# Kernel tuning notes

Measured on AMD Instinct MI355X. Metric: run time of the kernel, lower is better.

Reference implementation:

```python
import jax, jax.numpy as jnp
import numpy as np

B, T, N, D, C = 32, 256, 256, 1024, 80
SIM_THRESH = 0.7
MAX_AGE = 10
W_SIM, W_IOU = 0.7, 0.3


def setup_inputs() -> dict:
    key = jax.random.key(0)
    ks = jax.random.split(key, 8)
    track_memory = jax.random.normal(ks[0], (B, T, D), jnp.float32)
    track_boxes = jax.random.uniform(ks[1], (B, T, 4), jnp.float32, 0.05, 0.95)
    track_active = jax.random.bernoulli(ks[2], 0.9, (B, T))
    track_age = jax.random.randint(ks[3], (B, T), 0, 5, jnp.int32)
    track_hits = jax.random.randint(ks[4], (B, T), 1, 10, jnp.int32)
    det_boxes = jax.random.uniform(ks[5], (B, N, 4), jnp.float32, 0.05, 0.95)
    # correlate detections with tracks so cosine similarity exceeds the
    # matching threshold for many pairs and the greedy loop does real work
    det_memory = track_memory + 0.3 * jax.random.normal(ks[6], (B, N, D), jnp.float32)
    class_logits = jax.random.normal(ks[7], (B, N, C), jnp.float32)
    return {
        'track_memory': track_memory, 'track_boxes': track_boxes,
        'track_active': track_active, 'track_age': track_age,
        'track_hits': track_hits, 'det_boxes': det_boxes,
        'det_memory': det_memory, 'class_logits': class_logits,
    }


def _normalize(x):
    # matches F.normalize(dim=-1): x / max(||x||, eps)
    n = jnp.linalg.norm(x, axis=-1, keepdims=True)
    return x / jnp.maximum(n, 1e-12)


def _iou_matrix(tb, db):
    # tb [T,4], db [N,4], boxes in (cx, cy, w, h) format -> IoU [T,N]
    t_x1, t_y1 = tb[:, 0] - tb[:, 2] / 2, tb[:, 1] - tb[:, 3] / 2
    t_x2, t_y2 = tb[:, 0] + tb[:, 2] / 2, tb[:, 1] + tb[:, 3] / 2
    d_x1, d_y1 = db[:, 0] - db[:, 2] / 2, db[:, 1] - db[:, 3] / 2
    d_x2, d_y2 = db[:, 0] + db[:, 2] / 2, db[:, 1] + db[:, 3] / 2
    iw = jnp.clip(jnp.minimum(t_x2[:, None], d_x2[None, :]) - jnp.maximum(t_x1[:, None], d_x1[None, :]), 0.0)
    ih = jnp.clip(jnp.minimum(t_y2[:, None], d_y2[None, :]) - jnp.maximum(t_y1[:, None], d_y1[None, :]), 0.0)
    inter = iw * ih
    union = (tb[:, 2] * tb[:, 3])[:, None] + (db[:, 2] * db[:, 3])[None, :] - inter
    return inter / (union + 1e-6)


def _greedy_match(Cmat):
    # sequential greedy argmax matching, as in the torch while-loop.
    # returns match_det [T]: detection index matched to each track, -1 if none.
    Tn, Nn = Cmat.shape

    def step(carry, _):
        Cm, match_det = carry
        flat = Cm.reshape(-1)
        idx = jnp.argmax(flat)
        val = flat[idx]
        ok = val >= SIM_THRESH
        t = idx // Nn
        d = idx % Nn
        match_det = jnp.where(ok, match_det.at[t].set(d.astype(jnp.int32)), match_det)
        Cm = jnp.where(ok, Cm.at[t, :].set(-1.0).at[:, d].set(-1.0), Cm)
        return (Cm, match_det), None

    init = (Cmat, jnp.full((Tn,), -1, jnp.int32))
    (_, match_det), _ = jax.lax.scan(step, init, None, length=min(Tn, Nn))
    return match_det


def reference(track_memory, track_boxes, track_active, track_age, track_hits,
              det_boxes, det_memory, class_logits):
    # detection scores (computed in torch update(); not used downstream)
    scores = jnp.max(jax.nn.softmax(class_logits, axis=-1), axis=-1)  # [B,N]

    def per_batch(tm, tb, ta, age, hits, db, dm):
        sim = _normalize(tm) @ _normalize(dm).T            # [T,N] cosine sim
        iou = _iou_matrix(tb, db)                          # [T,N]
        Cmat = W_SIM * sim + W_IOU * iou
        Cmat = jnp.where(ta[:, None], Cmat, -1.0)          # inactive rows -> -1
        match_det = _greedy_match(Cmat)                    # [T]
        matched = match_det >= 0
        d = jnp.clip(match_det, 0)
        new_mem = jnp.where(matched[:, None], dm[d], tm)
        new_box = jnp.where(matched[:, None], db[d], tb)
        new_hits = jnp.where(matched, hits + 1, hits)
        unmatched_active = ta & ~matched
        new_age = jnp.where(matched, 0, jnp.where(unmatched_active, age + 1, age))
        new_active = jnp.where(matched, True,
                               jnp.where(unmatched_active, new_age <= MAX_AGE, ta))
        return new_mem, new_box, new_active, new_age, new_hits, match_det

    new_mem, new_box, new_active, new_age, new_hits, match_det = jax.vmap(per_batch)(
        track_memory, track_boxes, track_active, track_age, track_hits,
        det_boxes, det_memory)
    return new_mem, new_box, new_active, new_age, new_hits, match_det, scores
```

## Files before the change

### kernel.cpp

```cpp
#include <hip/hip_runtime.h>
#include <math.h>

static constexpr int PB = 32, PT = 256, PN = 256, PD = 1024, PC = 80;
static constexpr int BCAP = 96;
static constexpr int CAP  = 256;
static constexpr int NT   = 16;

static constexpr size_t O_MEM   = 0;
static constexpr size_t O_BOX   = O_MEM   + (size_t)PB*PT*PD;
static constexpr size_t O_ACT   = O_BOX   + (size_t)PB*PT*4;
static constexpr size_t O_AGE   = O_ACT   + (size_t)PB*PT;
static constexpr size_t O_HITS  = O_AGE   + (size_t)PB*PT;
static constexpr size_t O_MATCH = O_HITS  + (size_t)PB*PT;
static constexpr size_t O_SCORE = O_MATCH + (size_t)PB*PT;

typedef __attribute__((ext_vector_type(8))) short short8;
typedef __attribute__((ext_vector_type(4))) float f32x4;

__device__ __forceinline__ unsigned ordbits(float f) {
    unsigned b = __float_as_uint(f);
    return (b & 0x80000000u) ? ~b : (b | 0x80000000u);
}
__device__ __forceinline__ unsigned short f2bf(float f) {
    unsigned u = __float_as_uint(f);
    unsigned r = u + 0x7fffu + ((u >> 16) & 1u);
    return (unsigned short)(r >> 16);
}

__device__ __forceinline__ float box_cost(float sim, float4 bt, float4 bd) {
    float tX1 = bt.x - bt.z*0.5f, tX2 = bt.x + bt.z*0.5f;
    float tY1 = bt.y - bt.w*0.5f, tY2 = bt.y + bt.w*0.5f;
    float dX1 = bd.x - bd.z*0.5f, dX2 = bd.x + bd.z*0.5f;
    float dY1 = bd.y - bd.w*0.5f, dY2 = bd.y + bd.w*0.5f;
    float iw = fmaxf(fminf(tX2, dX2) - fmaxf(tX1, dX1), 0.f);
    float ih = fmaxf(fminf(tY2, dY2) - fmaxf(tY1, dY1), 0.f);
    float inter = iw * ih;
    float iou = inter / (bt.z*bt.w + bd.z*bd.w - inter + 1e-6f);
    return 0.7f * sim + 0.3f * iou;
}

__global__ __launch_bounds__(256) void k_prep(
        const float* __restrict__ tm, const float* __restrict__ dm,
        const float* __restrict__ lg,
        short* __restrict__ abf, short* __restrict__ bbf,
        float* __restrict__ asums, float* __restrict__ bsums,
        float* __restrict__ ddots, float* __restrict__ out) {
    const int bx = blockIdx.x;
    const int tid = threadIdx.x;
    const int w = tid >> 6, lane = tid & 63;
    if (bx < PB * PT / 4) {
        const size_t row = (size_t)bx * 4 + w;
        const float4* ap = (const float4*)(tm + row * PD);
        const float4* dp = (const float4*)(dm + row * PD);
        float4 a[4], d[4];
#pragma unroll
        for (int q = 0; q < 4; ++q) { a[q] = ap[lane + 64 * q]; d[q] = dp[lane + 64 * q]; }
        float as = 0.f, bs = 0.f, dd = 0.f;
        uint2 pa[4], pd2[4];
#pragma unroll
        for (int q = 0; q < 4; ++q) {
            as += a[q].x*a[q].x + a[q].y*a[q].y + a[q].z*a[q].z + a[q].w*a[q].w;
            bs += d[q].x*d[q].x + d[q].y*d[q].y + d[q].z*d[q].z + d[q].w*d[q].w;
            dd += a[q].x*d[q].x + a[q].y*d[q].y + a[q].z*d[q].z + a[q].w*d[q].w;
            pa[q].x  = f2bf(a[q].x) | ((unsigned)f2bf(a[q].y) << 16);
            pa[q].y  = f2bf(a[q].z) | ((unsigned)f2bf(a[q].w) << 16);
            pd2[q].x = f2bf(d[q].x) | ((unsigned)f2bf(d[q].y) << 16);
            pd2[q].y = f2bf(d[q].z) | ((unsigned)f2bf(d[q].w) << 16);
        }
        uint2* ao = (uint2*)(abf + row * PD);
        uint2* bo = (uint2*)(bbf + row * PD);
#pragma unroll
        for (int q = 0; q < 4; ++q) { ao[lane + 64 * q] = pa[q]; bo[lane + 64 * q] = pd2[q]; }
#pragma unroll
        for (int o = 1; o < 64; o <<= 1) {
            as += __shfl_xor(as, o);
            bs += __shfl_xor(bs, o);
            dd += __shfl_xor(dd, o);
        }
        if (lane == 0) {
            asums[row] = as;
            bsums[row] = bs;
            ddots[row] = dd;
        }
    } else {
        int rowi = (bx - PB * PT / 4) * 4 + w;
        const float* p = lg + (size_t)rowi * PC;
        float x0 = p[lane];
        float x1 = (lane < PC - 64) ? p[64 + lane] : -INFINITY;
        float m = fmaxf(x0, x1);
#pragma unroll
        for (int o = 32; o > 0; o >>= 1) m = fmaxf(m, __shfl_down(m, o));
        m = __shfl(m, 0);
        float s = expf(x0 - m) + ((lane < PC - 64) ? expf(x1 - m) : 0.f);
#pragma unroll
        for (int o = 32; o > 0; o >>= 1) s += __shfl_down(s, o);
        if (lane == 0) out[O_SCORE + rowi] = 1.0f / s;
    }
}

__global__ __launch_bounds__(256) void k_sim(
        const short* __restrict__ abf, const short* __restrict__ bbf,
        const float* __restrict__ tb, const float* __restrict__ db,
        const unsigned* __restrict__ ta,
        const float* __restrict__ asums, const float* __restrict__ bsums,
        unsigned* __restrict__ cntblk, int* __restrict__ cand) {
    const int b = blockIdx.z;
    const int rowbase = blockIdx.y * 64;
    const int colbase = blockIdx.x * 64;
    const int bid = b * NT + blockIdx.y * 4 + blockIdx.x;
    const int tid = threadIdx.x;
    const int w = tid >> 6, lane = tid & 63;
    const int wm = w >> 1, wn = w & 1;
    const int m16 = lane & 15, quad = lane >> 4;

    __shared__ unsigned bcnt;
    __shared__ float ainv[64], binv[64];
    if (tid == 0) bcnt = 0u;
    if (tid < 64)
        ainv[tid] = 1.0f / fmaxf(sqrtf(asums[b * PT + rowbase + tid]), 1e-12f);
    else if (tid < 128)
        binv[tid - 64] = 1.0f / fmaxf(sqrtf(bsums[b * PN + colbase + tid - 64]), 1e-12f);

    const short* Ab = abf + ((size_t)b * PT + rowbase) * PD;
    const short* Bb = bbf + ((size_t)b * PN + colbase) * PD;
    const short8* pA0 = (const short8*)(Ab + (size_t)(wm * 32 +      m16) * PD) + quad;
    const short8* pA1 = (const short8*)(Ab + (size_t)(wm * 32 + 16 + m16) * PD) + quad;
    const short8* pB0 = (const short8*)(Bb + (size_t)(wn * 32 +      m16) * PD) + quad;
    const short8* pB1 = (const short8*)(Bb + (size_t)(wn * 32 + 16 + m16) * PD) + quad;

    f32x4 acc00 = (f32x4)0.f, acc01 = (f32x4)0.f;
    f32x4 acc10 = (f32x4)0.f, acc11 = (f32x4)0.f;
#pragma unroll 8
    for (int kk = 0; kk < PD / 32; ++kk) {
        short8 a0 = pA0[kk * 4];
        short8 a1 = pA1[kk * 4];
        short8 b0 = pB0[kk * 4];
        short8 b1 = pB1[kk * 4];
        acc00 = __builtin_amdgcn_mfma_f32_16x16x32_bf16(a0, b0, acc00, 0, 0, 0);
        acc01 = __builtin_amdgcn_mfma_f32_16x16x32_bf16(a0, b1, acc01, 0, 0, 0);
        acc10 = __builtin_amdgcn_mfma_f32_16x16x32_bf16(a1, b0, acc10, 0, 0, 0);
        acc11 = __builtin_amdgcn_mfma_f32_16x16x32_bf16(a1, b1, acc11, 0, 0, 0);
    }
    f32x4 accm[2][2] = {{acc00, acc01}, {acc10, acc11}};

    __syncthreads();

    float dx1[2], dy1[2], dx2[2], dy2[2], darea[2], dnv[2];
    int ng[2];
#pragma unroll
    for (int nj = 0; nj < 2; ++nj) {
        int cl = wn * 32 + nj * 16 + m16;
        ng[nj] = colbase + cl;
        dnv[nj] = binv[cl];
        float4 bx = *(const float4*)&db[((size_t)b * PN + ng[nj]) * 4];
        dx1[nj] = bx.x - bx.z * 0.5f; dx2[nj] = bx.x + bx.z * 0.5f;
        dy1[nj] = bx.y - bx.w * 0.5f; dy2[nj] = bx.y + bx.w * 0.5f;
        darea[nj] = bx.z * bx.w;
    }

#pragma unroll
    for (int mi = 0; mi < 2; ++mi) {
#pragma unroll
        for (int r = 0; r < 4; ++r) {
            int tl = wm * 32 + mi * 16 + quad * 4 + r;
            int tg = rowbase + tl;
            if (ta[b * PT + tg] == 0u) continue;
            float tnv = ainv[tl];
            float4 bx = *(const float4*)&tb[((size_t)b * PT + tg) * 4];
            float tX1 = bx.x - bx.z * 0.5f, tX2 = bx.x + bx.z * 0.5f;
            float tY1 = bx.y - bx.w * 0.5f, tY2 = bx.y + bx.w * 0.5f;
            float tA = bx.z * bx.w;
#pragma unroll
            for (int nj = 0; nj < 2; ++nj) {
                float sim = accm[mi][nj][r] * tnv * dnv[nj];
                float iw = fmaxf(fminf(tX2, dx2[nj]) - fmaxf(tX1, dx1[nj]), 0.f);
                float ih = fmaxf(fminf(tY2, dy2[nj]) - fmaxf(tY1, dy1[nj]), 0.f);
                float inter = iw * ih;
                float iou = inter / (tA + darea[nj] - inter + 1e-6f);
                float cost = 0.7f * sim + 0.3f * iou;
                if (cost >= 0.695f) {
                    unsigned idx = atomicAdd(&bcnt, 1u);
                    if (idx < BCAP) cand[bid * BCAP + idx] = (tg << 8) | ng[nj];
                }
            }
        }
    }
    __syncthreads();
    if (tid == 0) cntblk[bid] = (bcnt > BCAP) ? BCAP : bcnt;
}

__global__ __launch_bounds__(256) void k_match(
        const float* __restrict__ tm, const float* __restrict__ dm,
        const float* __restrict__ tb, const float* __restrict__ db,
        const float* __restrict__ asums, const float* __restrict__ bsums,
        const float* __restrict__ ddots,
        const unsigned* __restrict__ cntblk, const int* __restrict__ cand,
        int* __restrict__ md) {
    const int b = blockIdx.x;
    const int tid = threadIdx.x;
    const int w = tid >> 6, lane = tid & 63;
    __shared__ int cnts[NT];
    __shared__ unsigned long long sel_key[CAP];
    __shared__ unsigned sel_cnt;
    __shared__ int odd_slot[64];
    __shared__ unsigned odd_cnt;
    __shared__ int rcnt[PT];
    __shared__ int ccnt[PN];
    __shared__ int conflict;

    if (tid == 0) { sel_cnt = 0u; odd_cnt = 0u; conflict = 0; }
    if (tid < NT) {
        int cj = (int)cntblk[b * NT + tid];
        cnts[tid] = (cj > BCAP) ? BCAP : cj;
    }
    rcnt[tid] = 0; ccnt[tid] = 0;
    md[b * PT + tid] = -1;
    __syncthreads();

    for (int u = tid; u < NT * BCAP; u += 256) {
        int j = u / BCAP, i = u - j * BCAP;
        if (i >= cnts[j]) continue;
        int gidx = (b * NT + j) * BCAP + i;
        int pair = cand[gidx];
        int t = pair >> 8, n = pair & 255;
        if (t == n) {
            float na  = asums[b * PT + t];
            float nb  = bsums[b * PN + n];
            float dot = ddots[b * PT + t];
            float sim = dot * (1.0f / fmaxf(sqrtf(na), 1e-12f))
                            * (1.0f / fmaxf(sqrtf(nb), 1e-12f));
            float4 bt = *(const float4*)&tb[((size_t)b * PT + t) * 4];
            float4 bd = *(const float4*)&db[((size_t)b * PN + n) * 4];
            float cost = box_cost(sim, bt, bd);
            if (cost >= 0.7f) {
                unsigned s = atomicAdd(&sel_cnt, 1u);
                if (s < CAP)
                    sel_key[s] = ((unsigned long long)ordbits(cost) << 16)
                               | (unsigned long long)(65535 - pair);
            }
        } else {
            unsigned oi = atomicAdd(&odd_cnt, 1u);
            if (oi < 64) odd_slot[oi] = gidx;
        }
    }
    __syncthreads();

    int nodd = (int)odd_cnt; if (nodd > 64) nodd = 64;
    for (int j = w; j < nodd; j += 4) {
        int pair = cand[odd_slot[j]];
        int t = pair >> 8, n = pair & 255;
        const float4* tr = (const float4*)(tm + ((size_t)b * PT + t) * PD);
        const float4* dr = (const float4*)(dm + ((size_t)b * PN + n) * PD);
        float dot = 0.f;
#pragma unroll
        for (int q = 0; q < 4; ++q) {
            float4 v = tr[lane + 64 * q];
            float4 u = dr[lane + 64 * q];
            dot += v.x*u.x + v.y*u.y + v.z*u.z + v.w*u.w;
        }
#pragma unroll
        for (int o = 1; o < 64; o <<= 1) dot += __shfl_xor(dot, o);
        if (lane == 0) {
            float na = asums[b * PT + t], nb = bsums[b * PN + n];
            float sim = dot * (1.0f / fmaxf(sqrtf(na), 1e-12f))
                            * (1.0f / fmaxf(sqrtf(nb), 1e-12f));
            float4 bt = *(const float4*)&tb[((size_t)b * PT + t) * 4];
            float4 bd = *(const float4*)&db[((size_t)b * PN + n) * 4];
            float cost = box_cost(sim, bt, bd);
            if (cost >= 0.7f) {
                unsigned s = atomicAdd(&sel_cnt, 1u);
                if (s < CAP)
                    sel_key[s] = ((unsigned long long)ordbits(cost) << 16)
                               | (unsigned long long)(65535 - pair);
            }
        }
    }
    __syncthreads();

    const unsigned ns = (sel_cnt > (unsigned)CAP) ? (unsigned)CAP : sel_cnt;
    for (unsigned s = tid; s < ns; s += 256) {
        int flat = 65535 - (int)(sel_key[s] & 0xFFFFull);
        if (atomicAdd(&rcnt[flat >> 8], 1) >= 1) conflict = 1;
        if (atomicAdd(&ccnt[flat & 255], 1) >= 1) conflict = 1;
    }
    __syncthreads();

    if (!conflict) {
        for (unsigned s = tid; s < ns; s += 256) {
            int flat = 65535 - (int)(sel_key[s] & 0xFFFFull);
            md[b * PT + (flat >> 8)] = flat & 255;
        }
        return;
    }

    if (w == 0) {
        unsigned long long k[4];
#pragma unroll
        for (int s = 0; s < 4; ++s) {
            unsigned idx = (unsigned)lane + 64u * s;
            k[s] = (idx < ns) ? sel_key[idx] : 0ull;
        }
        int mdv[4] = {-1, -1, -1, -1};
        for (int it = 0; it < PT; ++it) {
            unsigned long long m = k[0];
            if (k[1] > m) m = k[1];
            if (k[2] > m) m = k[2];
            if (k[3] > m) m = k[3];
#pragma unroll
            for (int o = 1; o < 64; o <<= 1) {
                unsigned long long s = __shfl_xor(m, o);
                if (s > m) m = s;
            }
            if (m == 0ull) break;
            int flat = 65535 - (int)(m & 0xFFFFull);
            int t = flat >> 8, d = flat & 255;
            if ((t & 63) == lane) mdv[t >> 6] = d;
#pragma unroll
            for (int s = 0; s < 4; ++s) {
                if (k[s]) {
                    int f2 = 65535 - (int)(k[s] & 0xFFFFull);
                    if ((f2 >> 8) == t || (f2 & 255) == d) k[s] = 0ull;
                }
            }
        }
#pragma unroll
        for (int s = 0; s < 4; ++s) md[b * PT + s * 64 + lane] = mdv[s];
    }
}

__global__ __launch_bounds__(256) void k_outsc(
        const float* __restrict__ tm, const float* __restrict__ tb,
        const unsigned* __restrict__ ta, const int* __restrict__ age,
        const int* __restrict__ hits, const float* __restrict__ db,
        const float* __restrict__ dm, const int* __restrict__ md,
        float* __restrict__ out) {
    const int w = threadIdx.x >> 6, lane = threadIdx.x & 63;
    int idx = blockIdx.x * 4 + w;
    int b = idx >> 8;
    int m = md[idx];
    bool matched = m >= 0;
    int d = matched ? m : 0;
    const float4* src = (const float4*)(matched ? dm + ((size_t)b * PN + d) * PD
                                                : tm + (size_t)idx * PD);
    float4* dst = (float4*)(out + O_MEM + (size_t)idx * PD);
#pragma unroll
    for (int q = 0; q < 4; ++q) dst[lane + 64 * q] = src[lane + 64 * q];
    if (lane < 4) {
        const float* sb = matched ? db + ((size_t)b * PN + d) * 4
                                  : tb + (size_t)idx * 4;
        out[O_BOX + (size_t)idx * 4 + lane] = sb[lane];
    }
    if (lane == 0) {
        bool tact = ta[idx] != 0u;
        int hh = hits[idx], ag = age[idx];
        int nh = matched ? hh + 1 : hh;
        bool unm = tact && !matched;
        int na = matched ? 0 : (unm ? ag + 1 : ag);
        bool nact = matched ? true : (unm ? (na <= 10) : tact);
        out[O_ACT   + idx] = nact ? 1.0f : 0.0f;
        out[O_AGE   + idx] = (float)na;
        out[O_HITS  + idx] = (float)nh;
        out[O_MATCH + idx] = (float)m;
    }
}

extern "C" void kernel_launch(void* const* d_in, const int* in_sizes, int n_in,
                              void* d_out, int out_size, void* d_ws, size_t ws_size,
                              hipStream_t stream) {
    const float*    tm   = (const float*)d_in[0];
    const float*    tb   = (const float*)d_in[1];
    const unsigned* ta   = (const unsigned*)d_in[2];
    const int*      age  = (const int*)d_in[3];
    const int*      hits = (const int*)d_in[4];
    const float*    db   = (const float*)d_in[5];
    const float*    dm   = (const float*)d_in[6];
    const float*    lg   = (const float*)d_in[7];
    float* out = (float*)d_out;

    char* ws = (char*)d_ws;
    short* abf   = (short*)ws;
    short* bbf   = abf + (size_t)PB * PT * PD;
    float* asums = (float*)(bbf + (size_t)PB * PN * PD);
    float* bsums = asums + PB * PT;
    float* ddots = bsums + PB * PN;
    unsigned* cntblk = (unsigned*)(ddots + PB * PT);
    int* cand = (int*)(cntblk + PB * NT);
    int* md   = cand + PB * NT * BCAP;

    k_prep <<<PB * PT / 4 + PB * PN / 4, 256, 0, stream>>>(
        tm, dm, lg, abf, bbf, asums, bsums, ddots, out);
    k_sim  <<<dim3(4, 4, PB), 256, 0, stream>>>(
        abf, bbf, tb, db, ta, asums, bsums, cntblk, cand);
    k_match<<<dim3(PB), 256, 0, stream>>>(
        tm, dm, tb, db, asums, bsums, ddots, cntblk, cand, md);
    k_outsc<<<PB * PT / 4, 256, 0, stream>>>(
        tm, tb, ta, age, hits, db, dm, md, out);
}
```

Baseline: 169.6 us.

## Store bf16 operands in MFMA fragment order and remap sim blocks per XCD

The prep kernel now writes the bf16 copies of track and detection memory pre-swizzled into 16-row MFMA fragment tiles, so each lane of k_sim reads a contiguous short8 and a wave's loads are fully coalesced instead of strided across rows. Row norms and dot products are reduced across waves through shared memory because each block now handles 16 rows. k_sim uses a 1D grid with batches mapped to XCDs so the tiles of one batch share an L2. This couples the prep and sim kernels to a fixed fragment layout and makes k_prep launch fewer, heavier blocks for that part.

```diff
diff --git a/kernel.cpp b/kernel.cpp
--- a/kernel.cpp
+++ b/kernel.cpp
@@ -17,6 +17,7 @@
 typedef __attribute__((ext_vector_type(8))) short short8;
 typedef __attribute__((ext_vector_type(4))) float f32x4;
 
+
 __device__ __forceinline__ unsigned ordbits(float f) {
     unsigned b = __float_as_uint(f);
     return (b & 0x80000000u) ? ~b : (b | 0x80000000u);
@@ -25,6 +26,14 @@
     unsigned u = __float_as_uint(f);
     unsigned r = u + 0x7fffu + ((u >> 16) & 1u);
     return (unsigned short)(r >> 16);
+}
+__device__ __forceinline__ short8 pack8(float4 lo, float4 hi) {
+    union { unsigned u[4]; short8 s; } r;
+    r.u[0] = f2bf(lo.x) | ((unsigned)f2bf(lo.y) << 16);
+    r.u[1] = f2bf(lo.z) | ((unsigned)f2bf(lo.w) << 16);
+    r.u[2] = f2bf(hi.x) | ((unsigned)f2bf(hi.y) << 16);
+    r.u[3] = f2bf(hi.z) | ((unsigned)f2bf(hi.w) << 16);
+    return r.s;
 }
 
 __device__ __forceinline__ float box_cost(float sim, float4 bt, float4 bd) {
@@ -48,42 +57,44 @@
     const int bx = blockIdx.x;
     const int tid = threadIdx.x;
     const int w = tid >> 6, lane = tid & 63;
-    if (bx < PB * PT / 4) {
-        const size_t row = (size_t)bx * 4 + w;
-        const float4* ap = (const float4*)(tm + row * PD);
-        const float4* dp = (const float4*)(dm + row * PD);
-        float4 a[4], d[4];
-#pragma unroll
-        for (int q = 0; q < 4; ++q) { a[q] = ap[lane + 64 * q]; d[q] = dp[lane + 64 * q]; }
+    if (bx < PB * PT / 16) {
+        const int m16 = lane & 15, quad = lane >> 4;
+        const int row = bx * 16 + m16;
+        const float* tp = tm + (size_t)row * PD;
+        const float* dp = dm + (size_t)row * PD;
+        const size_t fb = (size_t)bx * 32 * 512;
         float as = 0.f, bs = 0.f, dd = 0.f;
-        uint2 pa[4], pd2[4];
-#pragma unroll
-        for (int q = 0; q < 4; ++q) {
-            as += a[q].x*a[q].x + a[q].y*a[q].y + a[q].z*a[q].z + a[q].w*a[q].w;
-            bs += d[q].x*d[q].x + d[q].y*d[q].y + d[q].z*d[q].z + d[q].w*d[q].w;
-            dd += a[q].x*d[q].x + a[q].y*d[q].y + a[q].z*d[q].z + a[q].w*d[q].w;
-            pa[q].x  = f2bf(a[q].x) | ((unsigned)f2bf(a[q].y) << 16);
-            pa[q].y  = f2bf(a[q].z) | ((unsigned)f2bf(a[q].w) << 16);
-            pd2[q].x = f2bf(d[q].x) | ((unsigned)f2bf(d[q].y) << 16);
-            pd2[q].y = f2bf(d[q].z) | ((unsigned)f2bf(d[q].w) << 16);
-        }
-        uint2* ao = (uint2*)(abf + row * PD);
-        uint2* bo = (uint2*)(bbf + row * PD);
-#pragma unroll
-        for (int q = 0; q < 4; ++q) { ao[lane + 64 * q] = pa[q]; bo[lane + 64 * q] = pd2[q]; }
-#pragma unroll
-        for (int o = 1; o < 64; o <<= 1) {
-            as += __shfl_xor(as, o);
-            bs += __shfl_xor(bs, o);
-            dd += __shfl_xor(dd, o);
-        }
-        if (lane == 0) {
-            asums[row] = as;
-            bsums[row] = bs;
-            ddots[row] = dd;
+#pragma unroll
+        for (int kq = 0; kq < 8; ++kq) {
+            const int kk = w * 8 + kq;
+            const int e = kk * 32 + quad * 8;
+            float4 a0 = *(const float4*)(tp + e);
+            float4 a1 = *(const float4*)(tp + e + 4);
+            float4 d0 = *(const float4*)(dp + e);
+            float4 d1 = *(const float4*)(dp + e + 4);
+            as += a0.x*a0.x + a0.y*a0.y + a0.z*a0.z + a0.w*a0.w
+                + a1.x*a1.x + a1.y*a1.y + a1.z*a1.z + a1.w*a1.w;
+            bs += d0.x*d0.x + d0.y*d0.y + d0.z*d0.z + d0.w*d0.w
+                + d1.x*d1.x + d1.y*d1.y + d1.z*d1.z + d1.w*d1.w;
+            dd += a0.x*d0.x + a0.y*d0.y + a0.z*d0.z + a0.w*d0.w
+                + a1.x*d1.x + a1.y*d1.y + a1.z*d1.z + a1.w*d1.w;
+            *(short8*)(abf + fb + (size_t)kk * 512 + lane * 8) = pack8(a0, a1);
+            *(short8*)(bbf + fb + (size_t)kk * 512 + lane * 8) = pack8(d0, d1);
+        }
+        as += __shfl_xor(as, 16); as += __shfl_xor(as, 32);
+        bs += __shfl_xor(bs, 16); bs += __shfl_xor(bs, 32);
+        dd += __shfl_xor(dd, 16); dd += __shfl_xor(dd, 32);
+        __shared__ float red[3][4][16];
+        if (quad == 0) { red[0][w][m16] = as; red[1][w][m16] = bs; red[2][w][m16] = dd; }
+        __syncthreads();
+        if (tid < 16) {
+            int rg = bx * 16 + tid;
+            asums[rg] = red[0][0][tid] + red[0][1][tid] + red[0][2][tid] + red[0][3][tid];
+            bsums[rg] = red[1][0][tid] + red[1][1][tid] + red[1][2][tid] + red[1][3][tid];
+            ddots[rg] = red[2][0][tid] + red[2][1][tid] + red[2][2][tid] + red[2][3][tid];
         }
     } else {
-        int rowi = (bx - PB * PT / 4) * 4 + w;
+        int rowi = (bx - PB * PT / 16) * 4 + w;
         const float* p = lg + (size_t)rowi * PC;
         float x0 = p[lane];
         float x1 = (lane < PC - 64) ? p[64 + lane] : -INFINITY;
@@ -104,10 +115,13 @@
         const unsigned* __restrict__ ta,
         const float* __restrict__ asums, const float* __restrict__ bsums,
         unsigned* __restrict__ cntblk, int* __restrict__ cand) {
-    const int b = blockIdx.z;
-    const int rowbase = blockIdx.y * 64;
-    const int colbase = blockIdx.x * 64;
-    const int bid = b * NT + blockIdx.y * 4 + blockIdx.x;
+    const int i = blockIdx.x;
+    const int xcd = i & 7, j = i >> 3;
+    const int b = xcd * 4 + (j >> 4);
+    const int tile = j & 15;
+    const int rowbase = (tile >> 2) * 64;
+    const int colbase = (tile & 3) * 64;
+    const int bid = b * NT + tile;
     const int tid = threadIdx.x;
     const int w = tid >> 6, lane = tid & 63;
     const int wm = w >> 1, wn = w & 1;
@@ -121,21 +135,19 @@
     else if (tid < 128)
         binv[tid - 64] = 1.0f / fmaxf(sqrtf(bsums[b * PN + colbase + tid - 64]), 1e-12f);
 
-    const short* Ab = abf + ((size_t)b * PT + rowbase) * PD;
-    const short* Bb = bbf + ((size_t)b * PN + colbase) * PD;
-    const short8* pA0 = (const short8*)(Ab + (size_t)(wm * 32 +      m16) * PD) + quad;
-    const short8* pA1 = (const short8*)(Ab + (size_t)(wm * 32 + 16 + m16) * PD) + quad;
-    const short8* pB0 = (const short8*)(Bb + (size_t)(wn * 32 +      m16) * PD) + quad;
-    const short8* pB1 = (const short8*)(Bb + (size_t)(wn * 32 + 16 + m16) * PD) + quad;
+    const short8* A8 = (const short8*)abf;
+    const short8* B8 = (const short8*)bbf;
+    const size_t a0b = ((size_t)(b * 16 + (rowbase >> 4) + wm * 2)) * 2048 + lane;
+    const size_t b0b = ((size_t)(b * 16 + (colbase >> 4) + wn * 2)) * 2048 + lane;
 
     f32x4 acc00 = (f32x4)0.f, acc01 = (f32x4)0.f;
     f32x4 acc10 = (f32x4)0.f, acc11 = (f32x4)0.f;
-#pragma unroll 8
-    for (int kk = 0; kk < PD / 32; ++kk) {
-        short8 a0 = pA0[kk * 4];
-        short8 a1 = pA1[kk * 4];
-        short8 b0 = pB0[kk * 4];
-        short8 b1 = pB1[kk * 4];
+#pragma unroll 4
+    for (int kk = 0; kk < 32; ++kk) {
+        short8 a0 = A8[a0b + (size_t)kk * 64];
+        short8 a1 = A8[a0b + (size_t)kk * 64 + 2048];
+        short8 b0 = B8[b0b + (size_t)kk * 64];
+        short8 b1 = B8[b0b + (size_t)kk * 64 + 2048];
         acc00 = __builtin_amdgcn_mfma_f32_16x16x32_bf16(a0, b0, acc00, 0, 0, 0);
         acc01 = __builtin_amdgcn_mfma_f32_16x16x32_bf16(a0, b1, acc01, 0, 0, 0);
         acc10 = __builtin_amdgcn_mfma_f32_16x16x32_bf16(a1, b0, acc10, 0, 0, 0);
@@ -387,9 +399,9 @@
     int* cand = (int*)(cntblk + PB * NT);
     int* md   = cand + PB * NT * BCAP;
 
-    k_prep <<<PB * PT / 4 + PB * PN / 4, 256, 0, stream>>>(
+    k_prep <<<PB * PT / 16 + PB * PN / 4, 256, 0, stream>>>(
         tm, dm, lg, abf, bbf, asums, bsums, ddots, out);
-    k_sim  <<<dim3(4, 4, PB), 256, 0, stream>>>(
+    k_sim  <<<PB * NT, 256, 0, stream>>>(
         abf, bbf, tb, db, ta, asums, bsums, cntblk, cand);
     k_match<<<dim3(PB), 256, 0, stream>>>(
         tm, dm, tb, db, asums, bsums, ddots, cntblk, cand, md);
```

After: 155.9 us. 1.09x faster.
